# Kernel optimization log

Measured on AMD Instinct MI355X. Metric: run time of the kernel, lower is better.

The kernel has to match this reference:

```python
import jax, jax.numpy as jnp
import numpy as np

IN_F = 4096
OUT_F = 11008
B, S = 4, 2048

def setup_inputs() -> dict:
    key = jax.random.key(0)
    k1, k2, k3, k4 = jax.random.split(key, 4)
    x = jax.random.normal(k1, (B, S, IN_F), dtype=jnp.float16)
    # int8 quantized weights in [-127, 127]
    qweight = jax.random.randint(k2, (OUT_F, IN_F), -127, 128, dtype=jnp.int32).astype(jnp.int8)
    # per-output-channel scale: small positive values like max_abs/127
    scale = (jax.random.uniform(k3, (OUT_F,), dtype=jnp.float32) * 0.02 + 1e-4).astype(jnp.float16)
    bias = jax.random.normal(k4, (OUT_F,), dtype=jnp.float16)
    return {"x": x, "qweight": qweight, "scale": scale, "bias": bias}

def reference(x, qweight, scale, bias):
    # dequant matmul: y = (x @ W_q^T) * scale + bias, all in fp16 (act_dtype)
    x = x.astype(jnp.float16)
    w = qweight.astype(jnp.float16)          # [out, in]
    y = jnp.einsum('bsi,oi->bso', x, w)       # [B, S, out]
    y = y * scale + bias
    return y.astype(jnp.float16)
```

## Files before the change

### kernel.cpp

```cpp
#include <hip/hip_runtime.h>
#include <hip/hip_fp16.h>
#include <stdint.h>

#define M_DIM 8192
#define K_DIM 4096
#define N_DIM 11008


typedef _Float16 f16x8 __attribute__((ext_vector_type(8)));
typedef float f32x4 __attribute__((ext_vector_type(4)));

typedef const void __attribute__((address_space(1)))* gptr_t;
typedef void __attribute__((address_space(3)))* lptr_t;

__device__ __forceinline__ void async_load16(const void* g, void* l) {
    __builtin_amdgcn_global_load_lds((gptr_t)g, (lptr_t)l, 16, 0, 0);
}

__device__ __forceinline__ void tile_barrier() {
    __builtin_amdgcn_sched_barrier(0);
    asm volatile("s_waitcnt vmcnt(0)" ::: "memory");
    __builtin_amdgcn_s_barrier();
    __builtin_amdgcn_sched_barrier(0);
}

__global__ void sniff_kernel(const int* __restrict__ q, int* __restrict__ flag) {
    __shared__ int s;
    if (threadIdx.x == 0) s = 1;
    __syncthreads();
    int bad = 0;
#pragma unroll
    for (int i = 0; i < 16; ++i) {
        int v = q[threadIdx.x * 16 + i];
        if (v < -127 || v > 127) bad = 1;
    }
    if (bad) s = 0;
    __syncthreads();
    if (threadIdx.x == 0) flag[0] = s;
}

__global__ __launch_bounds__(256)
void cvt_x_kernel(const float* __restrict__ in, _Float16* __restrict__ out) {
    const size_t n8 = (size_t)M_DIM * K_DIM / 8;
    const size_t stride = (size_t)gridDim.x * 256;
    for (size_t i = (size_t)blockIdx.x * 256 + threadIdx.x; i < n8; i += stride) {
        const float4* p = (const float4*)(in + i * 8);
        float4 a = p[0], b = p[1];
        f16x8 h;
        h[0] = (_Float16)a.x; h[1] = (_Float16)a.y;
        h[2] = (_Float16)a.z; h[3] = (_Float16)a.w;
        h[4] = (_Float16)b.x; h[5] = (_Float16)b.y;
        h[6] = (_Float16)b.z; h[7] = (_Float16)b.w;
        *(f16x8*)(out + i * 8) = h;
    }
}

__global__ __launch_bounds__(256)
void cvt_w_kernel(const void* __restrict__ in, _Float16* __restrict__ out,
                  const int* __restrict__ flag) {
    const bool w_is_i32 = (flag[0] != 0);
    const size_t n8 = (size_t)N_DIM * K_DIM / 8;
    const size_t stride = (size_t)gridDim.x * 256;
    if (w_is_i32) {
        const int* q = (const int*)in;
        for (size_t i = (size_t)blockIdx.x * 256 + threadIdx.x; i < n8; i += stride) {
            const int4* p = (const int4*)(q + i * 8);
            int4 a = p[0], b = p[1];
            f16x8 h;
            h[0] = (_Float16)a.x; h[1] = (_Float16)a.y;
            h[2] = (_Float16)a.z; h[3] = (_Float16)a.w;
            h[4] = (_Float16)b.x; h[5] = (_Float16)b.y;
            h[6] = (_Float16)b.z; h[7] = (_Float16)b.w;
            *(f16x8*)(out + i * 8) = h;
        }
    } else {
        const signed char* q = (const signed char*)in;
        for (size_t i = (size_t)blockIdx.x * 256 + threadIdx.x; i < n8; i += stride) {
            const int2* p = (const int2*)(q + i * 8);
            int2 raw = p[0];
            f16x8 h;
            h[0] = (_Float16)(signed char)(raw.x & 0xff);
            h[1] = (_Float16)(signed char)((raw.x >> 8) & 0xff);
            h[2] = (_Float16)(signed char)((raw.x >> 16) & 0xff);
            h[3] = (_Float16)(signed char)((raw.x >> 24) & 0xff);
            h[4] = (_Float16)(signed char)(raw.y & 0xff);
            h[5] = (_Float16)(signed char)((raw.y >> 8) & 0xff);
            h[6] = (_Float16)(signed char)((raw.y >> 16) & 0xff);
            h[7] = (_Float16)(signed char)((raw.y >> 24) & 0xff);
            *(f16x8*)(out + i * 8) = h;
        }
    }
}

#define BM2 256
#define BN2 256
#define BK2 64
#define TM2 (M_DIM / BM2)
#define TN2 (N_DIM / BN2)
#define NWG2 (TM2 * TN2)

__global__ __launch_bounds__(512, 2)
void f16_gemm256_kernel(const _Float16* __restrict__ A,
                        const _Float16* __restrict__ W,
                        const float* __restrict__ scale,
                        const float* __restrict__ bias,
                        float* __restrict__ C)
{
    __shared__ __align__(16) _Float16 As[2 * BM2 * BK2];
    __shared__ __align__(16) _Float16 Bs[2 * BN2 * BK2];

    const int tid  = threadIdx.x;
    const int wave = tid >> 6;
    const int lane = tid & 63;
    const int quad = lane >> 4;
    const int col  = lane & 15;

    const int bid = blockIdx.x;
    const int xcd = bid & 7;
    const int r   = bid >> 3;
    const int bm  = xcd * 4 + r / TN2;
    const int bn  = r % TN2;

    const int m0 = bm * BM2;
    const int n0 = bn * BN2;
    const int wm = (wave >> 2) * 128;
    const int wn = (wave & 3) * 64;

    f32x4 acc[8][4];
#pragma unroll
    for (int i = 0; i < 8; ++i)
#pragma unroll
        for (int j = 0; j < 4; ++j)
            acc[i][j] = (f32x4){0.f, 0.f, 0.f, 0.f};

    const int srow   = tid >> 3;
    const int schunk = (tid & 7) ^ (srow & 7);
    const _Float16* ga = A + (size_t)(m0 + srow) * K_DIM + schunk * 8;
    const _Float16* gw = W + (size_t)(n0 + srow) * K_DIM + schunk * 8;

    const int cx0 = ((0 * 4 + quad) ^ (col & 7)) * 8;
    const int cx1 = ((1 * 4 + quad) ^ (col & 7)) * 8;

#pragma unroll
    for (int i = 0; i < 4; ++i) {
        async_load16(ga + (size_t)i * 64 * K_DIM, As + tid * 8 + i * 4096);
        async_load16(gw + (size_t)i * 64 * K_DIM, Bs + tid * 8 + i * 4096);
    }
    tile_barrier();

    const int NT = K_DIM / BK2;
#pragma unroll 2
    for (int t = 0; t < NT; ++t) {
        const int cur = t & 1;
        const _Float16* Ab = As + cur * (BM2 * BK2);
        const _Float16* Bb = Bs + cur * (BN2 * BK2);

        if (t + 1 < NT) {
            const int nxt = cur ^ 1;
            const int k1 = (t + 1) * BK2;
            _Float16* la = As + nxt * (BM2 * BK2) + tid * 8;
            _Float16* lb = Bs + nxt * (BN2 * BK2) + tid * 8;
#pragma unroll
            for (int i = 0; i < 4; ++i) {
                async_load16(ga + (size_t)i * 64 * K_DIM + k1, la + i * 4096);
                async_load16(gw + (size_t)i * 64 * K_DIM + k1, lb + i * 4096);
            }
        }

        f16x8 a[8], bq[8];
#pragma unroll
        for (int mi = 0; mi < 4; ++mi) {
            const _Float16* ap = Ab + (wm + mi * 16 + col) * BK2;
            a[mi * 2 + 0] = *(const f16x8*)(ap + cx0);
            a[mi * 2 + 1] = *(const f16x8*)(ap + cx1);
        }
#pragma unroll
        for (int ni = 0; ni < 2; ++ni) {
            const _Float16* bp = Bb + (wn + ni * 16 + col) * BK2;
            bq[ni * 2 + 0] = *(const f16x8*)(bp + cx0);
            bq[ni * 2 + 1] = *(const f16x8*)(bp + cx1);
        }
        __builtin_amdgcn_s_setprio(1);
#pragma unroll
        for (int mi = 0; mi < 4; ++mi)
#pragma unroll
            for (int ni = 0; ni < 2; ++ni) {
                acc[mi][ni] = __builtin_amdgcn_mfma_f32_16x16x32_f16(
                    a[mi * 2 + 0], bq[ni * 2 + 0], acc[mi][ni], 0, 0, 0);
                acc[mi][ni] = __builtin_amdgcn_mfma_f32_16x16x32_f16(
                    a[mi * 2 + 1], bq[ni * 2 + 1], acc[mi][ni], 0, 0, 0);
            }
        __builtin_amdgcn_s_setprio(0);

#pragma unroll
        for (int ni = 2; ni < 4; ++ni) {
            const _Float16* bp = Bb + (wn + ni * 16 + col) * BK2;
            bq[ni * 2 + 0] = *(const f16x8*)(bp + cx0);
            bq[ni * 2 + 1] = *(const f16x8*)(bp + cx1);
        }
        __builtin_amdgcn_s_setprio(1);
#pragma unroll
        for (int mi = 0; mi < 4; ++mi)
#pragma unroll
            for (int ni = 2; ni < 4; ++ni) {
                acc[mi][ni] = __builtin_amdgcn_mfma_f32_16x16x32_f16(
                    a[mi * 2 + 0], bq[ni * 2 + 0], acc[mi][ni], 0, 0, 0);
                acc[mi][ni] = __builtin_amdgcn_mfma_f32_16x16x32_f16(
                    a[mi * 2 + 1], bq[ni * 2 + 1], acc[mi][ni], 0, 0, 0);
            }
        __builtin_amdgcn_s_setprio(0);

#pragma unroll
        for (int mi = 0; mi < 4; ++mi) {
            const _Float16* ap = Ab + (wm + 64 + mi * 16 + col) * BK2;
            a[mi * 2 + 0] = *(const f16x8*)(ap + cx0);
            a[mi * 2 + 1] = *(const f16x8*)(ap + cx1);
        }
        __builtin_amdgcn_s_setprio(1);
#pragma unroll
        for (int mi = 0; mi < 4; ++mi)
#pragma unroll
            for (int ni = 0; ni < 2; ++ni) {
                acc[4 + mi][ni] = __builtin_amdgcn_mfma_f32_16x16x32_f16(
                    a[mi * 2 + 0], bq[ni * 2 + 0], acc[4 + mi][ni], 0, 0, 0);
                acc[4 + mi][ni] = __builtin_amdgcn_mfma_f32_16x16x32_f16(
                    a[mi * 2 + 1], bq[ni * 2 + 1], acc[4 + mi][ni], 0, 0, 0);
            }
        __builtin_amdgcn_s_setprio(0);

        __builtin_amdgcn_s_setprio(1);
#pragma unroll
        for (int mi = 0; mi < 4; ++mi)
#pragma unroll
            for (int ni = 2; ni < 4; ++ni) {
                acc[4 + mi][ni] = __builtin_amdgcn_mfma_f32_16x16x32_f16(
                    a[mi * 2 + 0], bq[ni * 2 + 0], acc[4 + mi][ni], 0, 0, 0);
                acc[4 + mi][ni] = __builtin_amdgcn_mfma_f32_16x16x32_f16(
                    a[mi * 2 + 1], bq[ni * 2 + 1], acc[4 + mi][ni], 0, 0, 0);
            }
        __builtin_amdgcn_s_setprio(0);

        tile_barrier();
    }

    float scl[4], bsv[4];
#pragma unroll
    for (int ni = 0; ni < 4; ++ni) {
        int n = n0 + wn + ni * 16 + col;
        scl[ni] = scale[n];
        bsv[ni] = bias[n];
    }
#pragma unroll
    for (int rh = 0; rh < 2; ++rh) {
#pragma unroll
        for (int mi = 0; mi < 4; ++mi) {
#pragma unroll
            for (int rr = 0; rr < 4; ++rr) {
                int m = m0 + wm + rh * 64 + mi * 16 + quad * 4 + rr;
                float* cp = C + (size_t)m * N_DIM + n0 + wn + col;
#pragma unroll
                for (int ni = 0; ni < 4; ++ni) {
                    cp[ni * 16] = acc[rh * 4 + mi][ni][rr] * scl[ni] + bsv[ni];
                }
            }
        }
    }
}

#define BM 128
#define BN 128
#define OBK 32
#define TM (M_DIM / BM)
#define TN (N_DIM / BN)

__global__ __launch_bounds__(256)
void w8_gemm_kernel(const float* __restrict__ A,
                    const void* __restrict__ Wv,
                    const float* __restrict__ scale,
                    const float* __restrict__ bias,
                    float* __restrict__ C,
                    const int* __restrict__ flag)
{
    __shared__ __align__(16) _Float16 As[BM * OBK];
    __shared__ __align__(16) _Float16 Bs[BN * OBK];

    const int tid  = threadIdx.x;
    const int wave = tid >> 6;
    const int lane = tid & 63;
    const int quad = lane >> 4;
    const int col  = lane & 15;

    const bool w_is_i32 = (flag[0] != 0);

    int bid = blockIdx.x;
    const int per_group = 8 * TN;
    int g = bid / per_group;
    int r = bid - g * per_group;
    const int bm = g * 8 + (r & 7);
    const int bn = r >> 3;

    const int m0 = bm * BM;
    const int n0 = bn * BN;
    const int wm = (wave >> 1) * 64;
    const int wn = (wave & 1) * 64;

    f32x4 acc[4][4];
#pragma unroll
    for (int mi = 0; mi < 4; ++mi)
#pragma unroll
        for (int ni = 0; ni < 4; ++ni)
            acc[mi][ni] = (f32x4){0.f, 0.f, 0.f, 0.f};

    for (int k0 = 0; k0 < K_DIM; k0 += OBK) {
#pragma unroll
        for (int i = 0; i < 2; ++i) {
            int idx = i * 256 + tid;
            int row = idx >> 2;
            int c   = idx & 3;
            const float4* p = (const float4*)(A + (size_t)(m0 + row) * K_DIM + k0 + c * 8);
            float4 v0 = p[0];
            float4 v1 = p[1];
            f16x8 h;
            h[0] = (_Float16)v0.x; h[1] = (_Float16)v0.y;
            h[2] = (_Float16)v0.z; h[3] = (_Float16)v0.w;
            h[4] = (_Float16)v1.x; h[5] = (_Float16)v1.y;
            h[6] = (_Float16)v1.z; h[7] = (_Float16)v1.w;
            *(f16x8*)(As + idx * 8) = h;
        }
        if (w_is_i32) {
            const int* Wq = (const int*)Wv;
#pragma unroll
            for (int i = 0; i < 2; ++i) {
                int idx = i * 256 + tid;
                int row = idx >> 2;
                int c   = idx & 3;
                const int4* p = (const int4*)(Wq + (size_t)(n0 + row) * K_DIM + k0 + c * 8);
                int4 a = p[0];
                int4 b = p[1];
                f16x8 h;
                h[0] = (_Float16)a.x; h[1] = (_Float16)a.y;
                h[2] = (_Float16)a.z; h[3] = (_Float16)a.w;
                h[4] = (_Float16)b.x; h[5] = (_Float16)b.y;
                h[6] = (_Float16)b.z; h[7] = (_Float16)b.w;
                *(f16x8*)(Bs + idx * 8) = h;
            }
        } else {
            const signed char* W8 = (const signed char*)Wv;
#pragma unroll
            for (int i = 0; i < 2; ++i) {
                int idx = i * 256 + tid;
                int row = idx >> 2;
                int c   = idx & 3;
                const int2* p = (const int2*)(W8 + (size_t)(n0 + row) * K_DIM + k0 + c * 8);
                int2 raw = p[0];
                f16x8 h;
                h[0] = (_Float16)(signed char)(raw.x & 0xff);
                h[1] = (_Float16)(signed char)((raw.x >> 8) & 0xff);
                h[2] = (_Float16)(signed char)((raw.x >> 16) & 0xff);
                h[3] = (_Float16)(signed char)((raw.x >> 24) & 0xff);
                h[4] = (_Float16)(signed char)(raw.y & 0xff);
                h[5] = (_Float16)(signed char)((raw.y >> 8) & 0xff);
                h[6] = (_Float16)(signed char)((raw.y >> 16) & 0xff);
                h[7] = (_Float16)(signed char)((raw.y >> 24) & 0xff);
                *(f16x8*)(Bs + idx * 8) = h;
            }
        }
        __syncthreads();

        f16x8 af[4], bfr[4];
#pragma unroll
        for (int mi = 0; mi < 4; ++mi)
            af[mi] = *(const f16x8*)(As + (wm + mi * 16 + col) * OBK + quad * 8);
#pragma unroll
        for (int ni = 0; ni < 4; ++ni)
            bfr[ni] = *(const f16x8*)(Bs + (wn + ni * 16 + col) * OBK + quad * 8);
#pragma unroll
        for (int mi = 0; mi < 4; ++mi)
#pragma unroll
            for (int ni = 0; ni < 4; ++ni)
                acc[mi][ni] = __builtin_amdgcn_mfma_f32_16x16x32_f16(
                    af[mi], bfr[ni], acc[mi][ni], 0, 0, 0);
        __syncthreads();
    }

    float scl[4], bs[4];
#pragma unroll
    for (int ni = 0; ni < 4; ++ni) {
        int n = n0 + wn + ni * 16 + col;
        scl[ni] = scale[n];
        bs[ni]  = bias[n];
    }
#pragma unroll
    for (int mi = 0; mi < 4; ++mi) {
#pragma unroll
        for (int rr = 0; rr < 4; ++rr) {
            int m = m0 + wm + mi * 16 + quad * 4 + rr;
            float* cp = C + (size_t)m * N_DIM + n0 + wn + col;
#pragma unroll
            for (int ni = 0; ni < 4; ++ni) {
                cp[ni * 16] = acc[mi][ni][rr] * scl[ni] + bs[ni];
            }
        }
    }
}

extern "C" void kernel_launch(void* const* d_in, const int* in_sizes, int n_in,
                              void* d_out, int out_size, void* d_ws, size_t ws_size,
                              hipStream_t stream) {
    const float* x     = (const float*)d_in[0];
    const void*  qw    = d_in[1];
    const float* scale = (const float*)d_in[2];
    const float* bias  = (const float*)d_in[3];
    float* out = (float*)d_out;

    int* flag = (int*)d_ws;

    const size_t A_BYTES = (size_t)M_DIM * K_DIM * 2;
    const size_t W_BYTES = (size_t)N_DIM * K_DIM * 2;
    const size_t NEED    = 256 + A_BYTES + W_BYTES;

    sniff_kernel<<<1, 256, 0, stream>>>((const int*)qw, flag);

    if (ws_size >= NEED) {
        _Float16* Ah = (_Float16*)((char*)d_ws + 256);
        _Float16* Wh = (_Float16*)((char*)d_ws + 256 + A_BYTES);
        cvt_x_kernel<<<2048, 256, 0, stream>>>(x, Ah);
        cvt_w_kernel<<<2048, 256, 0, stream>>>(qw, Wh, flag);
        f16_gemm256_kernel<<<NWG2, 512, 0, stream>>>(Ah, Wh, scale, bias, out);
    } else {
        w8_gemm_kernel<<<TM * TN, 256, 0, stream>>>(x, qw, scale, bias, out, flag);
    }
}
```

Before: 1.261 ms.

## Split next-tile async loads into staged groups with partial vmcnt waits

Replaces the single per-tile bulk prefetch and full vmcnt(0) barrier with four staged pairs of global-to-LDS loads interleaved between MFMA phases. Each phase waits with vmcnt(4) so that only older load groups must land, and the B tile row mapping is reorganized to match the staged order. The aim is to spread memory issue across the K-step and overlap load latency with compute. The cost is more barriers per iteration, and the last iteration issues redundant wrapped-around loads.

```diff
diff --git a/kernel.cpp b/kernel.cpp
--- a/kernel.cpp
+++ b/kernel.cpp
@@ -17,9 +17,15 @@
     __builtin_amdgcn_global_load_lds((gptr_t)g, (lptr_t)l, 16, 0, 0);
 }
 
-__device__ __forceinline__ void tile_barrier() {
+__device__ __forceinline__ void wait4_barrier() {
     __builtin_amdgcn_sched_barrier(0);
-    asm volatile("s_waitcnt vmcnt(0)" ::: "memory");
+    asm volatile("s_waitcnt vmcnt(4)" ::: "memory");
+    __builtin_amdgcn_s_barrier();
+    __builtin_amdgcn_sched_barrier(0);
+}
+__device__ __forceinline__ void plain_barrier() {
+    __builtin_amdgcn_sched_barrier(0);
+    asm volatile("" ::: "memory");
     __builtin_amdgcn_s_barrier();
     __builtin_amdgcn_sched_barrier(0);
 }
@@ -98,6 +104,7 @@
 #define TM2 (M_DIM / BM2)
 #define TN2 (N_DIM / BN2)
 #define NWG2 (TM2 * TN2)
+#define BUFE (BM2 * BK2)
 
 __global__ __launch_bounds__(512, 2)
 void f16_gemm256_kernel(const _Float16* __restrict__ A,
@@ -106,8 +113,8 @@
                         const float* __restrict__ bias,
                         float* __restrict__ C)
 {
-    __shared__ __align__(16) _Float16 As[2 * BM2 * BK2];
-    __shared__ __align__(16) _Float16 Bs[2 * BN2 * BK2];
+    __shared__ __align__(16) _Float16 As[2 * BUFE];
+    __shared__ __align__(16) _Float16 Bs[2 * BUFE];
 
     const int tid  = threadIdx.x;
     const int wave = tid >> 6;
@@ -133,52 +140,57 @@
         for (int j = 0; j < 4; ++j)
             acc[i][j] = (f32x4){0.f, 0.f, 0.f, 0.f};
 
-    const int srow   = tid >> 3;
-    const int schunk = (tid & 7) ^ (srow & 7);
-    const _Float16* ga = A + (size_t)(m0 + srow) * K_DIM + schunk * 8;
-    const _Float16* gw = W + (size_t)(n0 + srow) * K_DIM + schunk * 8;
+    const int tq     = tid >> 3;
+    const int c8     = (tid & 7) * 8;
+    const int schunk = (tid & 7) ^ (tq & 7);
+    const _Float16* gA = A + (size_t)(m0 + tq) * K_DIM + schunk * 8;
+    const int br0 = ((tq >> 5) << 6) + (tq & 31);
+    const _Float16* gB = W + (size_t)(n0 + br0) * K_DIM + schunk * 8;
+    const int la0 = tid * 8;
+    const int lb0 = br0 * 64 + c8;
 
     const int cx0 = ((0 * 4 + quad) ^ (col & 7)) * 8;
     const int cx1 = ((1 * 4 + quad) ^ (col & 7)) * 8;
 
-#pragma unroll
-    for (int i = 0; i < 4; ++i) {
-        async_load16(ga + (size_t)i * 64 * K_DIM, As + tid * 8 + i * 4096);
-        async_load16(gw + (size_t)i * 64 * K_DIM, Bs + tid * 8 + i * 4096);
-    }
-    tile_barrier();
+    {
+        _Float16* An = As;
+        _Float16* Bn = Bs;
+        async_load16(gA,                            An + la0);
+        async_load16(gA + (size_t)128 * K_DIM,      An + 8192 + la0);
+        async_load16(gB,                            Bn + lb0);
+        async_load16(gB + (size_t)128 * K_DIM,      Bn + 8192 + lb0);
+        async_load16(gB + (size_t)32 * K_DIM,       Bn + 2048 + lb0);
+        async_load16(gB + (size_t)160 * K_DIM,      Bn + 10240 + lb0);
+        async_load16(gA + (size_t)64 * K_DIM,       An + 4096 + la0);
+        async_load16(gA + (size_t)192 * K_DIM,      An + 12288 + la0);
+    }
+    wait4_barrier();
 
     const int NT = K_DIM / BK2;
 #pragma unroll 2
     for (int t = 0; t < NT; ++t) {
         const int cur = t & 1;
-        const _Float16* Ab = As + cur * (BM2 * BK2);
-        const _Float16* Bb = Bs + cur * (BN2 * BK2);
-
-        if (t + 1 < NT) {
-            const int nxt = cur ^ 1;
-            const int k1 = (t + 1) * BK2;
-            _Float16* la = As + nxt * (BM2 * BK2) + tid * 8;
-            _Float16* lb = Bs + nxt * (BN2 * BK2) + tid * 8;
-#pragma unroll
-            for (int i = 0; i < 4; ++i) {
-                async_load16(ga + (size_t)i * 64 * K_DIM + k1, la + i * 4096);
-                async_load16(gw + (size_t)i * 64 * K_DIM + k1, lb + i * 4096);
-            }
-        }
-
-        f16x8 a[8], bq[8];
+        const _Float16* Ab = As + cur * BUFE;
+        const _Float16* Bb = Bs + cur * BUFE;
+        _Float16* An = As + (cur ^ 1) * BUFE;
+        _Float16* Bn = Bs + (cur ^ 1) * BUFE;
+        const int kk = ((t + 1) & (NT - 1)) * BK2;
+
+        f16x8 alo[8], ba[4], bb[4], ahi[8];
+
+        async_load16(gA + kk,                       An + la0);
+        async_load16(gA + (size_t)128 * K_DIM + kk, An + 8192 + la0);
 #pragma unroll
         for (int mi = 0; mi < 4; ++mi) {
             const _Float16* ap = Ab + (wm + mi * 16 + col) * BK2;
-            a[mi * 2 + 0] = *(const f16x8*)(ap + cx0);
-            a[mi * 2 + 1] = *(const f16x8*)(ap + cx1);
+            alo[mi * 2 + 0] = *(const f16x8*)(ap + cx0);
+            alo[mi * 2 + 1] = *(const f16x8*)(ap + cx1);
         }
 #pragma unroll
         for (int ni = 0; ni < 2; ++ni) {
             const _Float16* bp = Bb + (wn + ni * 16 + col) * BK2;
-            bq[ni * 2 + 0] = *(const f16x8*)(bp + cx0);
-            bq[ni * 2 + 1] = *(const f16x8*)(bp + cx1);
+            ba[ni * 2 + 0] = *(const f16x8*)(bp + cx0);
+            ba[ni * 2 + 1] = *(const f16x8*)(bp + cx1);
         }
         __builtin_amdgcn_s_setprio(1);
 #pragma unroll
@@ -186,35 +198,41 @@
 #pragma unroll
             for (int ni = 0; ni < 2; ++ni) {
                 acc[mi][ni] = __builtin_amdgcn_mfma_f32_16x16x32_f16(
-                    a[mi * 2 + 0], bq[ni * 2 + 0], acc[mi][ni], 0, 0, 0);
+                    alo[mi * 2 + 0], ba[ni * 2 + 0], acc[mi][ni], 0, 0, 0);
                 acc[mi][ni] = __builtin_amdgcn_mfma_f32_16x16x32_f16(
-                    a[mi * 2 + 1], bq[ni * 2 + 1], acc[mi][ni], 0, 0, 0);
+                    alo[mi * 2 + 1], ba[ni * 2 + 1], acc[mi][ni], 0, 0, 0);
             }
         __builtin_amdgcn_s_setprio(0);
-
-#pragma unroll
-        for (int ni = 2; ni < 4; ++ni) {
-            const _Float16* bp = Bb + (wn + ni * 16 + col) * BK2;
-            bq[ni * 2 + 0] = *(const f16x8*)(bp + cx0);
-            bq[ni * 2 + 1] = *(const f16x8*)(bp + cx1);
+        wait4_barrier();
+
+        async_load16(gB + kk,                       Bn + lb0);
+        async_load16(gB + (size_t)128 * K_DIM + kk, Bn + 8192 + lb0);
+#pragma unroll
+        for (int ni = 0; ni < 2; ++ni) {
+            const _Float16* bp = Bb + (wn + 32 + ni * 16 + col) * BK2;
+            bb[ni * 2 + 0] = *(const f16x8*)(bp + cx0);
+            bb[ni * 2 + 1] = *(const f16x8*)(bp + cx1);
         }
         __builtin_amdgcn_s_setprio(1);
 #pragma unroll
         for (int mi = 0; mi < 4; ++mi)
 #pragma unroll
-            for (int ni = 2; ni < 4; ++ni) {
-                acc[mi][ni] = __builtin_amdgcn_mfma_f32_16x16x32_f16(
-                    a[mi * 2 + 0], bq[ni * 2 + 0], acc[mi][ni], 0, 0, 0);
-                acc[mi][ni] = __builtin_amdgcn_mfma_f32_16x16x32_f16(
-                    a[mi * 2 + 1], bq[ni * 2 + 1], acc[mi][ni], 0, 0, 0);
+            for (int ni = 0; ni < 2; ++ni) {
+                acc[mi][2 + ni] = __builtin_amdgcn_mfma_f32_16x16x32_f16(
+                    alo[mi * 2 + 0], bb[ni * 2 + 0], acc[mi][2 + ni], 0, 0, 0);
+                acc[mi][2 + ni] = __builtin_amdgcn_mfma_f32_16x16x32_f16(
+                    alo[mi * 2 + 1], bb[ni * 2 + 1], acc[mi][2 + ni], 0, 0, 0);
             }
         __builtin_amdgcn_s_setprio(0);
-
+        wait4_barrier();
+
+        async_load16(gB + (size_t)32 * K_DIM + kk,  Bn + 2048 + lb0);
+        async_load16(gB + (size_t)160 * K_DIM + kk, Bn + 10240 + lb0);
 #pragma unroll
         for (int mi = 0; mi < 4; ++mi) {
             const _Float16* ap = Ab + (wm + 64 + mi * 16 + col) * BK2;
-            a[mi * 2 + 0] = *(const f16x8*)(ap + cx0);
-            a[mi * 2 + 1] = *(const f16x8*)(ap + cx1);
+            ahi[mi * 2 + 0] = *(const f16x8*)(ap + cx0);
+            ahi[mi * 2 + 1] = *(const f16x8*)(ap + cx1);
         }
         __builtin_amdgcn_s_setprio(1);
 #pragma unroll
@@ -222,26 +240,29 @@
 #pragma unroll
             for (int ni = 0; ni < 2; ++ni) {
                 acc[4 + mi][ni] = __builtin_amdgcn_mfma_f32_16x16x32_f16(
-                    a[mi * 2 + 0], bq[ni * 2 + 0], acc[4 + mi][ni], 0, 0, 0);
+                    ahi[mi * 2 + 0], ba[ni * 2 + 0], acc[4 + mi][ni], 0, 0, 0);
                 acc[4 + mi][ni] = __builtin_amdgcn_mfma_f32_16x16x32_f16(
-                    a[mi * 2 + 1], bq[ni * 2 + 1], acc[4 + mi][ni], 0, 0, 0);
+                    ahi[mi * 2 + 1], ba[ni * 2 + 1], acc[4 + mi][ni], 0, 0, 0);
             }
         __builtin_amdgcn_s_setprio(0);
-
+        plain_barrier();
+
+        async_load16(gA + (size_t)64 * K_DIM + kk,  An + 4096 + la0);
+        async_load16(gA + (size_t)192 * K_DIM + kk, An + 12288 + la0);
         __builtin_amdgcn_s_setprio(1);
 #pragma unroll
         for (int mi = 0; mi < 4; ++mi)
 #pragma unroll
-            for (int ni = 2; ni < 4; ++ni) {
-                acc[4 + mi][ni] = __builtin_amdgcn_mfma_f32_16x16x32_f16(
-                    a[mi * 2 + 0], bq[ni * 2 + 0], acc[4 + mi][ni], 0, 0, 0);
-                acc[4 + mi][ni] = __builtin_amdgcn_mfma_f32_16x16x32_f16(
-                    a[mi * 2 + 1], bq[ni * 2 + 1], acc[4 + mi][ni], 0, 0, 0);
+            for (int ni = 0; ni < 2; ++ni) {
+                acc[4 + mi][2 + ni] = __builtin_amdgcn_mfma_f32_16x16x32_f16(
+                    ahi[mi * 2 + 0], bb[ni * 2 + 0], acc[4 + mi][2 + ni], 0, 0, 0);
+                acc[4 + mi][2 + ni] = __builtin_amdgcn_mfma_f32_16x16x32_f16(
+                    ahi[mi * 2 + 1], bb[ni * 2 + 1], acc[4 + mi][2 + ni], 0, 0, 0);
             }
         __builtin_amdgcn_s_setprio(0);
-
-        tile_barrier();
-    }
+        wait4_barrier();
+    }
+    asm volatile("s_waitcnt vmcnt(0)" ::: "memory");
 
     float scl[4], bsv[4];
 #pragma unroll
```

New measurement: 1.242 ms. About the same (-1.5%).
